# Kernel optimization log

Measured on AMD Instinct MI355X. Metric: run time of the kernel, lower is better.

## Reference

```python
import jax, jax.numpy as jnp
import numpy as np

B, S, D, H = 2, 2048, 1024, 16
HD = D // H


def setup_inputs() -> dict:
    key = jax.random.key(0)
    ks = jax.random.split(key, 9)
    x = jax.random.normal(ks[0], (B, S, D), dtype=jnp.float32)
    scale = 1.0 / np.sqrt(D)
    Wq = jax.random.normal(ks[1], (D, D), dtype=jnp.float32) * scale
    bq = jnp.zeros((D,), dtype=jnp.float32)
    Wk = jax.random.normal(ks[2], (D, D), dtype=jnp.float32) * scale
    bk = jnp.zeros((D,), dtype=jnp.float32)
    Wv = jax.random.normal(ks[3], (D, D), dtype=jnp.float32) * scale
    bv = jnp.zeros((D,), dtype=jnp.float32)
    Wo = jax.random.normal(ks[4], (D, D), dtype=jnp.float32) * scale
    bo = jnp.zeros((D,), dtype=jnp.float32)
    return {"x": x, "Wq": Wq, "bq": bq, "Wk": Wk, "bk": bk,
            "Wv": Wv, "bv": bv, "Wo": Wo, "bo": bo}


def reference(x, Wq, bq, Wk, bk, Wv, bv, Wo, bo):
    b, s, d = x.shape
    h, hd = H, HD
    # torch Linear: y = x @ W.T + b
    q = (x @ Wq.T + bq).reshape(b, s, h, hd).transpose(0, 2, 1, 3)  # (b,h,s,hd)
    k = (x @ Wk.T + bk).reshape(b, s, h, hd).transpose(0, 2, 1, 3)
    v = (x @ Wv.T + bv).reshape(b, s, h, hd).transpose(0, 2, 1, 3)
    scores = jnp.einsum('bhqd,bhkd->bhqk', q, k) / np.sqrt(hd)  # (b,h,s,s)
    # FAITHFUL to source: softmax over dim=1 (head axis), not the key axis.
    attn = jax.nn.softmax(scores, axis=1)
    # dropout is identity at inference
    out = jnp.einsum('bhqk,bhkd->bhqd', attn, v)  # (b,h,s,hd)
    out = out.transpose(0, 2, 1, 3).reshape(b, s, d)
    return out @ Wo.T + bo
```

## Files before the change

kernel.cpp:

```cpp
#include <hip/hip_runtime.h>
#include <hip/hip_bf16.h>
#include <cstdint>
#include <cstddef>


typedef __bf16 bf16x8 __attribute__((ext_vector_type(8)));
typedef __bf16 bf16x4 __attribute__((ext_vector_type(4)));
typedef _Float16 f16x4 __attribute__((ext_vector_type(4)));
typedef _Float16 f16x8 __attribute__((ext_vector_type(8)));
typedef float floatx4 __attribute__((ext_vector_type(4)));

#define S_LEN 2048
#define DIM 1024
#define NH 16
#define HD 64
#define MTOT 4096

__device__ __forceinline__ void g2l16(const void* g, void* l) {
    __builtin_amdgcn_global_load_lds(
        (const __attribute__((address_space(1))) void*)g,
        (__attribute__((address_space(3))) void*)l, 16, 0, 0);
}

__global__ void cast_f32_bf16(const float* __restrict__ s, __bf16* __restrict__ d, int n) {
    int i = (blockIdx.x * blockDim.x + threadIdx.x) * 4;
    if (i < n) {
        float4 v = *(const float4*)&s[i];
        bf16x4 o;
        o.x = (__bf16)v.x; o.y = (__bf16)v.y; o.z = (__bf16)v.z; o.w = (__bf16)v.w;
        *(bf16x4*)&d[i] = o;
    }
}

__global__ void cast_w4(const float* __restrict__ w0, const float* __restrict__ w1,
                        const float* __restrict__ w2, const float* __restrict__ w3,
                        __bf16* __restrict__ o0, __bf16* __restrict__ o1,
                        __bf16* __restrict__ o2, __bf16* __restrict__ o3, int n) {
    const float* s; __bf16* d;
    switch (blockIdx.y) {
        case 0: s = w0; d = o0; break;
        case 1: s = w1; d = o1; break;
        case 2: s = w2; d = o2; break;
        default: s = w3; d = o3; break;
    }
    int i = (blockIdx.x * blockDim.x + threadIdx.x) * 4;
    if (i < n) {
        float4 v = *(const float4*)&s[i];
        bf16x4 o;
        o.x = (__bf16)v.x; o.y = (__bf16)v.y; o.z = (__bf16)v.z; o.w = (__bf16)v.w;
        *(bf16x4*)&d[i] = o;
    }
}

__global__ __launch_bounds__(256, 4) void qkv_gemm(const __bf16* __restrict__ A,
                                                   const __bf16* __restrict__ Wq,
                                                   const __bf16* __restrict__ Wk,
                                                   const __bf16* __restrict__ Wv,
                                                   const float* __restrict__ bq,
                                                   const float* __restrict__ bk,
                                                   const float* __restrict__ bv,
                                                   __bf16* __restrict__ Qo,
                                                   __bf16* __restrict__ Ko,
                                                   _Float16* __restrict__ Vt) {
    const int tng = blockIdx.x * 64, tm = blockIdx.y * 128;
    const int wsel = tng >> 10, tn = tng & 1023;
    const __bf16* W = (wsel == 0) ? Wq : (wsel == 1) ? Wk : Wv;
    const float* bias = (wsel == 0) ? bq : (wsel == 1) ? bk : bv;
    __shared__ __bf16 As[2 * 128 * 32];
    __shared__ __bf16 Bs[2 * 64 * 32];
    const int tid = threadIdx.x, wid = tid >> 6, lane = tid & 63;
    const int l15 = lane & 15, quad = lane >> 4;
    const int wm = (wid >> 1) * 64, wn = (wid & 1) * 32;
    floatx4 acc[4][2] = {};
    for (int k0 = 0; k0 < DIM; k0 += 64) {
        __syncthreads();
#pragma unroll
        for (int i = 0; i < 4; ++i) {
            int slot = i * 256 + tid;
            int p = slot >> 9, r = (slot >> 2) & 127, c8 = (slot & 3) * 8;
            g2l16(&A[(size_t)(tm + r) * DIM + k0 + p * 32 + c8], &As[slot * 8]);
        }
#pragma unroll
        for (int i = 0; i < 2; ++i) {
            int slot = i * 256 + tid;
            int p = slot >> 8, r = (slot >> 2) & 63, c8 = (slot & 3) * 8;
            g2l16(&W[(size_t)(tn + r) * DIM + k0 + p * 32 + c8], &Bs[slot * 8]);
        }
        __syncthreads();
#pragma unroll
        for (int kc = 0; kc < 2; ++kc) {
            bf16x8 af[4], bf[2];
#pragma unroll
            for (int t = 0; t < 4; ++t)
                af[t] = *(const bf16x8*)&As[kc * 4096 + (wm + t * 16 + l15) * 32 + quad * 8];
#pragma unroll
            for (int t = 0; t < 2; ++t)
                bf[t] = *(const bf16x8*)&Bs[kc * 2048 + (wn + t * 16 + l15) * 32 + quad * 8];
#pragma unroll
            for (int im = 0; im < 4; ++im)
#pragma unroll
                for (int in = 0; in < 2; ++in)
                    acc[im][in] = __builtin_amdgcn_mfma_f32_16x16x32_bf16(af[im], bf[in], acc[im][in], 0, 0, 0);
        }
    }
    if (wsel < 2) {
        __bf16* O = wsel ? Ko : Qo;
#pragma unroll
        for (int im = 0; im < 4; ++im)
#pragma unroll
            for (int in = 0; in < 2; ++in)
#pragma unroll
                for (int r = 0; r < 4; ++r) {
                    int row = tm + wm + im * 16 + quad * 4 + r;
                    int col = tn + wn + in * 16 + l15;
                    O[(size_t)row * DIM + col] = (__bf16)(acc[im][in][r] + bias[col]);
                }
    } else {
#pragma unroll
        for (int im = 0; im < 4; ++im)
#pragma unroll
            for (int in = 0; in < 2; ++in) {
                int cv = tn + wn + in * 16 + l15;
                int row4 = tm + wm + im * 16 + quad * 4;
                float bv_ = bias[cv];
                f16x4 o;
#pragma unroll
                for (int r = 0; r < 4; ++r) o[r] = (_Float16)(acc[im][in][r] + bv_);
                *(f16x4*)&Vt[(size_t)cv * MTOT + row4] = o;
            }
    }
}

__global__ __launch_bounds__(256, 2) void gemm_out(const __bf16* __restrict__ A,
                                                   const __bf16* __restrict__ Bw,
                                                   const float* __restrict__ bias,
                                                   float* __restrict__ C) {
    const int tm = blockIdx.y * 128, tn = blockIdx.x * 64;
    __shared__ __bf16 As[2 * 128 * 32];
    __shared__ __bf16 Bs[2 * 64 * 32];
    const int tid = threadIdx.x, wid = tid >> 6, lane = tid & 63;
    const int l15 = lane & 15, quad = lane >> 4;
    const int wm = (wid >> 1) * 64, wn = (wid & 1) * 32;
    floatx4 acc[4][2] = {};
    for (int k0 = 0; k0 < DIM; k0 += 64) {
        __syncthreads();
#pragma unroll
        for (int i = 0; i < 4; ++i) {
            int slot = i * 256 + tid;
            int p = slot >> 9, r = (slot >> 2) & 127, c8 = (slot & 3) * 8;
            g2l16(&A[(size_t)(tm + r) * DIM + k0 + p * 32 + c8], &As[slot * 8]);
        }
#pragma unroll
        for (int i = 0; i < 2; ++i) {
            int slot = i * 256 + tid;
            int p = slot >> 8, r = (slot >> 2) & 63, c8 = (slot & 3) * 8;
            g2l16(&Bw[(size_t)(tn + r) * DIM + k0 + p * 32 + c8], &Bs[slot * 8]);
        }
        __syncthreads();
#pragma unroll
        for (int kc = 0; kc < 2; ++kc) {
            bf16x8 af[4], bf[2];
#pragma unroll
            for (int t = 0; t < 4; ++t)
                af[t] = *(const bf16x8*)&As[kc * 4096 + (wm + t * 16 + l15) * 32 + quad * 8];
#pragma unroll
            for (int t = 0; t < 2; ++t)
                bf[t] = *(const bf16x8*)&Bs[kc * 2048 + (wn + t * 16 + l15) * 32 + quad * 8];
#pragma unroll
            for (int im = 0; im < 4; ++im)
#pragma unroll
                for (int in = 0; in < 2; ++in)
                    acc[im][in] = __builtin_amdgcn_mfma_f32_16x16x32_bf16(af[im], bf[in], acc[im][in], 0, 0, 0);
        }
    }
#pragma unroll
    for (int im = 0; im < 4; ++im)
#pragma unroll
        for (int in = 0; in < 2; ++in)
#pragma unroll
            for (int r = 0; r < 4; ++r) {
                int row = tm + wm + im * 16 + quad * 4 + r;
                int col = tn + wn + in * 16 + l15;
                C[(size_t)row * DIM + col] = acc[im][in][r] + bias[col];
            }
}

__global__ __launch_bounds__(256, 4) void den3(const __bf16* __restrict__ Q,
                                               const __bf16* __restrict__ Km,
                                               __bf16* __restrict__ rd) {
    const int kt = blockIdx.x * 128, qt = blockIdx.y * 64, b = blockIdx.z;
    __shared__ __bf16 Ks[2 * 2 * 128 * 32];
    const int tid = threadIdx.x, wid = tid >> 6, lane = tid & 63;
    const int l15 = lane & 15, quad = lane >> 4;
    const int wq = wid * 16;
    floatx4 dsum[8] = {};
    const size_t qrow = (size_t)(b * S_LEN + qt + wq + l15) * DIM;
    for (int hh = 0; hh < 8; ++hh) {
        __syncthreads();
#pragma unroll
        for (int i = 0; i < 8; ++i) {
            int slot = i * 256 + tid;
            int hs = slot >> 10, rem = slot & 1023;
            int p = rem >> 9, r = (rem >> 2) & 127, c8 = (rem & 3) * 8;
            g2l16(&Km[(size_t)(b * S_LEN + kt + r) * DIM + (hh * 2 + hs) * HD + p * 32 + c8],
                  &Ks[slot * 8]);
        }
        __syncthreads();
#pragma unroll
        for (int hs = 0; hs < 2; ++hs) {
            int h = hh * 2 + hs;
            bf16x8 af0 = *(const bf16x8*)&Q[qrow + h * HD + quad * 8];
            bf16x8 af1 = *(const bf16x8*)&Q[qrow + h * HD + 32 + quad * 8];
#pragma unroll
            for (int n = 0; n < 8; ++n) {
                bf16x8 b0 = *(const bf16x8*)&Ks[hs * 8192 + (n * 16 + l15) * 32 + quad * 8];
                bf16x8 b1 = *(const bf16x8*)&Ks[hs * 8192 + 4096 + (n * 16 + l15) * 32 + quad * 8];
                floatx4 acc = {};
                acc = __builtin_amdgcn_mfma_f32_16x16x32_bf16(af0, b0, acc, 0, 0, 0);
                acc = __builtin_amdgcn_mfma_f32_16x16x32_bf16(af1, b1, acc, 0, 0, 0);
#pragma unroll
                for (int r = 0; r < 4; ++r) dsum[n][r] += __expf(acc[r] * 0.125f);
            }
        }
    }
#pragma unroll
    for (int n = 0; n < 8; ++n)
#pragma unroll
        for (int r = 0; r < 4; ++r) {
            int q = qt + wq + quad * 4 + r;
            int k = kt + n * 16 + l15;
            rd[(size_t)(b * S_LEN + q) * S_LEN + k] = (__bf16)(1.0f / dsum[n][r]);
        }
}

__global__ __launch_bounds__(256, 4) void attn3(const __bf16* __restrict__ Q,
                                                const __bf16* __restrict__ Km,
                                                const _Float16* __restrict__ Vt,
                                                const __bf16* __restrict__ rd,
                                                __bf16* __restrict__ AO) {
    const int qt = blockIdx.x * 64, h = blockIdx.y, b = blockIdx.z;
    __shared__ __bf16 Ks[2 * 128 * 32];
    __shared__ _Float16 Vts[64 * 136];
    const int tid = threadIdx.x, wid = tid >> 6, lane = tid & 63;
    const int l15 = lane & 15, quad = lane >> 4;
    const int wq = wid * 16;
    const size_t qrow = (size_t)(b * S_LEN + qt + wq + l15) * DIM + h * HD;
    bf16x8 qf0 = *(const bf16x8*)&Q[qrow + quad * 8];
    bf16x8 qf1 = *(const bf16x8*)&Q[qrow + 32 + quad * 8];
    const __bf16* rdrow = &rd[(size_t)(b * S_LEN + qt + wq + l15) * S_LEN];
    floatx4 oacc[4] = {};
    for (int kt = 0; kt < S_LEN; kt += 128) {
        __syncthreads();
#pragma unroll
        for (int i = 0; i < 4; ++i) {
            int slot = i * 256 + tid;
            int p = slot >> 9, r = (slot >> 2) & 127, c8 = (slot & 3) * 8;
            g2l16(&Km[(size_t)(b * S_LEN + kt + r) * DIM + h * HD + p * 32 + c8], &Ks[slot * 8]);
        }
#pragma unroll
        for (int i = 0; i < 4; ++i) {
            int slot = i * 256 + tid;
            int r = slot >> 4, c = (slot & 15) * 8;
            *(f16x8*)&Vts[r * 136 + c] =
                *(const f16x8*)&Vt[(size_t)(h * HD + r) * MTOT + b * S_LEN + kt + c];
        }
        __syncthreads();
#pragma unroll
        for (int mp = 0; mp < 8; ++mp) {
            bf16x8 kf0 = *(const bf16x8*)&Ks[(mp * 16 + l15) * 32 + quad * 8];
            bf16x8 kf1 = *(const bf16x8*)&Ks[4096 + (mp * 16 + l15) * 32 + quad * 8];
            floatx4 s = {};
            s = __builtin_amdgcn_mfma_f32_16x16x32_bf16(kf0, qf0, s, 0, 0, 0);
            s = __builtin_amdgcn_mfma_f32_16x16x32_bf16(kf1, qf1, s, 0, 0, 0);
            bf16x4 rv = *(const bf16x4*)&rdrow[kt + mp * 16 + quad * 4];
            f16x4 pa;
#pragma unroll
            for (int r = 0; r < 4; ++r)
                pa[r] = (_Float16)(__expf(s[r] * 0.125f) * (float)rv[r]);
#pragma unroll
            for (int n = 0; n < 4; ++n) {
                f16x4 vb = *(const f16x4*)&Vts[(n * 16 + l15) * 136 + mp * 16 + quad * 4];
                oacc[n] = __builtin_amdgcn_mfma_f32_16x16x16f16(pa, vb, oacc[n], 0, 0, 0);
            }
        }
    }
#pragma unroll
    for (int n = 0; n < 4; ++n)
#pragma unroll
        for (int r = 0; r < 4; ++r) {
            int row = qt + wq + quad * 4 + r;
            int col = h * HD + n * 16 + l15;
            AO[(size_t)(b * S_LEN + row) * DIM + col] = (__bf16)oacc[n][r];
        }
}

extern "C" void kernel_launch(void* const* d_in, const int* in_sizes, int n_in,
                              void* d_out, int out_size, void* d_ws, size_t ws_size,
                              hipStream_t stream) {
    const float* x  = (const float*)d_in[0];
    const float* Wq = (const float*)d_in[1];
    const float* bq = (const float*)d_in[2];
    const float* Wk = (const float*)d_in[3];
    const float* bk = (const float*)d_in[4];
    const float* Wv = (const float*)d_in[5];
    const float* bv = (const float*)d_in[6];
    const float* Wo = (const float*)d_in[7];
    const float* bo = (const float*)d_in[8];
    float* out = (float*)d_out;

    char* ws = (char*)d_ws;
    const size_t MB = 1u << 20;
    __bf16*    xb  = (__bf16*)(ws);
    __bf16*    Wqb = (__bf16*)(ws + 8 * MB);
    __bf16*    Wkb = (__bf16*)(ws + 10 * MB);
    __bf16*    Wvb = (__bf16*)(ws + 12 * MB);
    __bf16*    Wob = (__bf16*)(ws + 14 * MB);
    __bf16*    Qb  = (__bf16*)(ws + 16 * MB);
    __bf16*    Kb  = (__bf16*)(ws + 24 * MB);
    _Float16*  VtH = (_Float16*)(ws + 32 * MB);
    __bf16*    rd  = (__bf16*)(ws + 40 * MB);
    __bf16*    AOb = (__bf16*)(ws + 56 * MB);

    cast_f32_bf16<<<4096, 256, 0, stream>>>(x, xb, MTOT * DIM);
    cast_w4<<<dim3(1024, 4), 256, 0, stream>>>(Wq, Wk, Wv, Wo, Wqb, Wkb, Wvb, Wob, DIM * DIM);

    qkv_gemm<<<dim3(48, 32), 256, 0, stream>>>(xb, Wqb, Wkb, Wvb, bq, bk, bv, Qb, Kb, VtH);

    den3<<<dim3(S_LEN / 128, S_LEN / 64, 2), 256, 0, stream>>>(Qb, Kb, rd);

    attn3<<<dim3(S_LEN / 64, NH, 2), 256, 0, stream>>>(Qb, Kb, VtH, rd, AOb);

    gemm_out<<<dim3(DIM / 64, MTOT / 128), 256, 0, stream>>>(AOb, Wob, bo, out);
}
```

Baseline: 282.4 us.

## Split attention over key halves, retile GEMMs, use exp2, fp16 output projection

```diff
diff --git a/kernel.cpp b/kernel.cpp
--- a/kernel.cpp
+++ b/kernel.cpp
@@ -15,6 +15,9 @@
 #define NH 16
 #define HD 64
 #define MTOT 4096
+#define C_EXP 0.1803368801111244f
+
+__device__ __forceinline__ float fast_exp2(float x) { return __builtin_amdgcn_exp2f(x); }
 
 __device__ __forceinline__ void g2l16(const void* g, void* l) {
     __builtin_amdgcn_global_load_lds(
@@ -35,24 +38,29 @@
 __global__ void cast_w4(const float* __restrict__ w0, const float* __restrict__ w1,
                         const float* __restrict__ w2, const float* __restrict__ w3,
                         __bf16* __restrict__ o0, __bf16* __restrict__ o1,
-                        __bf16* __restrict__ o2, __bf16* __restrict__ o3, int n) {
+                        __bf16* __restrict__ o2, _Float16* __restrict__ o3, int n) {
+    int i = (blockIdx.x * blockDim.x + threadIdx.x) * 4;
+    if (i >= n) return;
+    if (blockIdx.y == 3) {
+        float4 v = *(const float4*)&w3[i];
+        f16x4 o;
+        o[0] = (_Float16)v.x; o[1] = (_Float16)v.y; o[2] = (_Float16)v.z; o[3] = (_Float16)v.w;
+        *(f16x4*)&o3[i] = o;
+        return;
+    }
     const float* s; __bf16* d;
     switch (blockIdx.y) {
         case 0: s = w0; d = o0; break;
         case 1: s = w1; d = o1; break;
-        case 2: s = w2; d = o2; break;
-        default: s = w3; d = o3; break;
-    }
-    int i = (blockIdx.x * blockDim.x + threadIdx.x) * 4;
-    if (i < n) {
-        float4 v = *(const float4*)&s[i];
-        bf16x4 o;
-        o.x = (__bf16)v.x; o.y = (__bf16)v.y; o.z = (__bf16)v.z; o.w = (__bf16)v.w;
-        *(bf16x4*)&d[i] = o;
-    }
-}
-
-__global__ __launch_bounds__(256, 4) void qkv_gemm(const __bf16* __restrict__ A,
+        default: s = w2; d = o2; break;
+    }
+    float4 v = *(const float4*)&s[i];
+    bf16x4 o;
+    o.x = (__bf16)v.x; o.y = (__bf16)v.y; o.z = (__bf16)v.z; o.w = (__bf16)v.w;
+    *(bf16x4*)&d[i] = o;
+}
+
+__global__ __launch_bounds__(256, 2) void qkv_gemm(const __bf16* __restrict__ A,
                                                    const __bf16* __restrict__ Wq,
                                                    const __bf16* __restrict__ Wk,
                                                    const __bf16* __restrict__ Wv,
@@ -62,53 +70,44 @@
                                                    __bf16* __restrict__ Qo,
                                                    __bf16* __restrict__ Ko,
                                                    _Float16* __restrict__ Vt) {
-    const int tng = blockIdx.x * 64, tm = blockIdx.y * 128;
+    const int tng = blockIdx.x * 128, tm = blockIdx.y * 128;
     const int wsel = tng >> 10, tn = tng & 1023;
     const __bf16* W = (wsel == 0) ? Wq : (wsel == 1) ? Wk : Wv;
     const float* bias = (wsel == 0) ? bq : (wsel == 1) ? bk : bv;
-    __shared__ __bf16 As[2 * 128 * 32];
-    __shared__ __bf16 Bs[2 * 64 * 32];
+    __shared__ __bf16 As[128 * 32];
+    __shared__ __bf16 Bs[128 * 32];
     const int tid = threadIdx.x, wid = tid >> 6, lane = tid & 63;
     const int l15 = lane & 15, quad = lane >> 4;
-    const int wm = (wid >> 1) * 64, wn = (wid & 1) * 32;
-    floatx4 acc[4][2] = {};
-    for (int k0 = 0; k0 < DIM; k0 += 64) {
-        __syncthreads();
-#pragma unroll
-        for (int i = 0; i < 4; ++i) {
-            int slot = i * 256 + tid;
-            int p = slot >> 9, r = (slot >> 2) & 127, c8 = (slot & 3) * 8;
-            g2l16(&A[(size_t)(tm + r) * DIM + k0 + p * 32 + c8], &As[slot * 8]);
-        }
+    const int wm = (wid >> 1) * 64, wn = (wid & 1) * 64;
+    floatx4 acc[4][4] = {};
+    for (int k0 = 0; k0 < DIM; k0 += 32) {
+        __syncthreads();
 #pragma unroll
         for (int i = 0; i < 2; ++i) {
             int slot = i * 256 + tid;
-            int p = slot >> 8, r = (slot >> 2) & 63, c8 = (slot & 3) * 8;
-            g2l16(&W[(size_t)(tn + r) * DIM + k0 + p * 32 + c8], &Bs[slot * 8]);
-        }
-        __syncthreads();
-#pragma unroll
-        for (int kc = 0; kc < 2; ++kc) {
-            bf16x8 af[4], bf[2];
-#pragma unroll
-            for (int t = 0; t < 4; ++t)
-                af[t] = *(const bf16x8*)&As[kc * 4096 + (wm + t * 16 + l15) * 32 + quad * 8];
-#pragma unroll
-            for (int t = 0; t < 2; ++t)
-                bf[t] = *(const bf16x8*)&Bs[kc * 2048 + (wn + t * 16 + l15) * 32 + quad * 8];
-#pragma unroll
-            for (int im = 0; im < 4; ++im)
-#pragma unroll
-                for (int in = 0; in < 2; ++in)
-                    acc[im][in] = __builtin_amdgcn_mfma_f32_16x16x32_bf16(af[im], bf[in], acc[im][in], 0, 0, 0);
-        }
+            int r = slot >> 2, c8 = (slot & 3) * 8;
+            g2l16(&A[(size_t)(tm + r) * DIM + k0 + c8], &As[slot * 8]);
+            g2l16(&W[(size_t)(tn + r) * DIM + k0 + c8], &Bs[slot * 8]);
+        }
+        __syncthreads();
+        bf16x8 af[4], bf[4];
+#pragma unroll
+        for (int t = 0; t < 4; ++t) {
+            af[t] = *(const bf16x8*)&As[(wm + t * 16 + l15) * 32 + quad * 8];
+            bf[t] = *(const bf16x8*)&Bs[(wn + t * 16 + l15) * 32 + quad * 8];
+        }
+#pragma unroll
+        for (int im = 0; im < 4; ++im)
+#pragma unroll
+            for (int in = 0; in < 4; ++in)
+                acc[im][in] = __builtin_amdgcn_mfma_f32_16x16x32_bf16(af[im], bf[in], acc[im][in], 0, 0, 0);
     }
     if (wsel < 2) {
         __bf16* O = wsel ? Ko : Qo;
 #pragma unroll
         for (int im = 0; im < 4; ++im)
 #pragma unroll
-            for (int in = 0; in < 2; ++in)
+            for (int in = 0; in < 4; ++in)
 #pragma unroll
                 for (int r = 0; r < 4; ++r) {
                     int row = tm + wm + im * 16 + quad * 4 + r;
@@ -119,7 +118,7 @@
 #pragma unroll
         for (int im = 0; im < 4; ++im)
 #pragma unroll
-            for (int in = 0; in < 2; ++in) {
+            for (int in = 0; in < 4; ++in) {
                 int cv = tn + wn + in * 16 + l15;
                 int row4 = tm + wm + im * 16 + quad * 4;
                 float bv_ = bias[cv];
@@ -131,77 +130,24 @@
     }
 }
 
-__global__ __launch_bounds__(256, 2) void gemm_out(const __bf16* __restrict__ A,
-                                                   const __bf16* __restrict__ Bw,
-                                                   const float* __restrict__ bias,
-                                                   float* __restrict__ C) {
-    const int tm = blockIdx.y * 128, tn = blockIdx.x * 64;
-    __shared__ __bf16 As[2 * 128 * 32];
-    __shared__ __bf16 Bs[2 * 64 * 32];
-    const int tid = threadIdx.x, wid = tid >> 6, lane = tid & 63;
-    const int l15 = lane & 15, quad = lane >> 4;
-    const int wm = (wid >> 1) * 64, wn = (wid & 1) * 32;
-    floatx4 acc[4][2] = {};
-    for (int k0 = 0; k0 < DIM; k0 += 64) {
-        __syncthreads();
-#pragma unroll
-        for (int i = 0; i < 4; ++i) {
-            int slot = i * 256 + tid;
-            int p = slot >> 9, r = (slot >> 2) & 127, c8 = (slot & 3) * 8;
-            g2l16(&A[(size_t)(tm + r) * DIM + k0 + p * 32 + c8], &As[slot * 8]);
-        }
-#pragma unroll
-        for (int i = 0; i < 2; ++i) {
-            int slot = i * 256 + tid;
-            int p = slot >> 8, r = (slot >> 2) & 63, c8 = (slot & 3) * 8;
-            g2l16(&Bw[(size_t)(tn + r) * DIM + k0 + p * 32 + c8], &Bs[slot * 8]);
-        }
-        __syncthreads();
-#pragma unroll
-        for (int kc = 0; kc < 2; ++kc) {
-            bf16x8 af[4], bf[2];
-#pragma unroll
-            for (int t = 0; t < 4; ++t)
-                af[t] = *(const bf16x8*)&As[kc * 4096 + (wm + t * 16 + l15) * 32 + quad * 8];
-#pragma unroll
-            for (int t = 0; t < 2; ++t)
-                bf[t] = *(const bf16x8*)&Bs[kc * 2048 + (wn + t * 16 + l15) * 32 + quad * 8];
-#pragma unroll
-            for (int im = 0; im < 4; ++im)
-#pragma unroll
-                for (int in = 0; in < 2; ++in)
-                    acc[im][in] = __builtin_amdgcn_mfma_f32_16x16x32_bf16(af[im], bf[in], acc[im][in], 0, 0, 0);
-        }
-    }
-#pragma unroll
-    for (int im = 0; im < 4; ++im)
-#pragma unroll
-        for (int in = 0; in < 2; ++in)
-#pragma unroll
-            for (int r = 0; r < 4; ++r) {
-                int row = tm + wm + im * 16 + quad * 4 + r;
-                int col = tn + wn + in * 16 + l15;
-                C[(size_t)row * DIM + col] = acc[im][in][r] + bias[col];
-            }
-}
-
-__global__ __launch_bounds__(256, 4) void den3(const __bf16* __restrict__ Q,
+__global__ __launch_bounds__(256, 8) void den4(const __bf16* __restrict__ Q,
                                                const __bf16* __restrict__ Km,
                                                __bf16* __restrict__ rd) {
-    const int kt = blockIdx.x * 128, qt = blockIdx.y * 64, b = blockIdx.z;
-    __shared__ __bf16 Ks[2 * 2 * 128 * 32];
+    const int kt = blockIdx.x * 64, qt = blockIdx.y * 64, b = blockIdx.z;
+    __shared__ __bf16 Ks[2 * 2 * 64 * 32];
     const int tid = threadIdx.x, wid = tid >> 6, lane = tid & 63;
     const int l15 = lane & 15, quad = lane >> 4;
     const int wq = wid * 16;
-    floatx4 dsum[8] = {};
+    floatx4 dsum[4] = {};
     const size_t qrow = (size_t)(b * S_LEN + qt + wq + l15) * DIM;
     for (int hh = 0; hh < 8; ++hh) {
         __syncthreads();
 #pragma unroll
-        for (int i = 0; i < 8; ++i) {
-            int slot = i * 256 + tid;
-            int hs = slot >> 10, rem = slot & 1023;
-            int p = rem >> 9, r = (rem >> 2) & 127, c8 = (rem & 3) * 8;
+        for (int i = 0; i < 4; ++i) {
+            int slot = i * 256 + tid;
+            int hs = slot >> 9, rem = slot & 511;
+            int p = rem >> 8, rem2 = rem & 255;
+            int r = rem2 >> 2, c8 = (rem2 & 3) * 8;
             g2l16(&Km[(size_t)(b * S_LEN + kt + r) * DIM + (hh * 2 + hs) * HD + p * 32 + c8],
                   &Ks[slot * 8]);
         }
@@ -212,19 +158,19 @@
             bf16x8 af0 = *(const bf16x8*)&Q[qrow + h * HD + quad * 8];
             bf16x8 af1 = *(const bf16x8*)&Q[qrow + h * HD + 32 + quad * 8];
 #pragma unroll
-            for (int n = 0; n < 8; ++n) {
-                bf16x8 b0 = *(const bf16x8*)&Ks[hs * 8192 + (n * 16 + l15) * 32 + quad * 8];
-                bf16x8 b1 = *(const bf16x8*)&Ks[hs * 8192 + 4096 + (n * 16 + l15) * 32 + quad * 8];
+            for (int n = 0; n < 4; ++n) {
+                bf16x8 b0 = *(const bf16x8*)&Ks[hs * 4096 + (n * 16 + l15) * 32 + quad * 8];
+                bf16x8 b1 = *(const bf16x8*)&Ks[hs * 4096 + 2048 + (n * 16 + l15) * 32 + quad * 8];
                 floatx4 acc = {};
                 acc = __builtin_amdgcn_mfma_f32_16x16x32_bf16(af0, b0, acc, 0, 0, 0);
                 acc = __builtin_amdgcn_mfma_f32_16x16x32_bf16(af1, b1, acc, 0, 0, 0);
 #pragma unroll
-                for (int r = 0; r < 4; ++r) dsum[n][r] += __expf(acc[r] * 0.125f);
-            }
-        }
-    }
-#pragma unroll
-    for (int n = 0; n < 8; ++n)
+                for (int r = 0; r < 4; ++r) dsum[n][r] += fast_exp2(acc[r] * C_EXP);
+            }
+        }
+    }
+#pragma unroll
+    for (int n = 0; n < 4; ++n)
 #pragma unroll
         for (int r = 0; r < 4; ++r) {
             int q = qt + wq + quad * 4 + r;
@@ -233,14 +179,16 @@
         }
 }
 
-__global__ __launch_bounds__(256, 4) void attn3(const __bf16* __restrict__ Q,
+__global__ __launch_bounds__(256, 8) void attn4(const __bf16* __restrict__ Q,
                                                 const __bf16* __restrict__ Km,
                                                 const _Float16* __restrict__ Vt,
                                                 const __bf16* __restrict__ rd,
-                                                __bf16* __restrict__ AO) {
-    const int qt = blockIdx.x * 64, h = blockIdx.y, b = blockIdx.z;
-    __shared__ __bf16 Ks[2 * 128 * 32];
-    __shared__ _Float16 Vts[64 * 136];
+                                                _Float16* __restrict__ AO1,
+                                                _Float16* __restrict__ AO2) {
+    const int qt = (blockIdx.x >> 1) * 64, ks = blockIdx.x & 1;
+    const int h = blockIdx.y, b = blockIdx.z;
+    __shared__ __bf16 Ks[2 * 64 * 32];
+    __shared__ _Float16 Vts[64 * 72];
     const int tid = threadIdx.x, wid = tid >> 6, lane = tid & 63;
     const int l15 = lane & 15, quad = lane >> 4;
     const int wq = wid * 16;
@@ -249,26 +197,28 @@
     bf16x8 qf1 = *(const bf16x8*)&Q[qrow + 32 + quad * 8];
     const __bf16* rdrow = &rd[(size_t)(b * S_LEN + qt + wq + l15) * S_LEN];
     floatx4 oacc[4] = {};
-    for (int kt = 0; kt < S_LEN; kt += 128) {
-        __syncthreads();
-#pragma unroll
-        for (int i = 0; i < 4; ++i) {
-            int slot = i * 256 + tid;
-            int p = slot >> 9, r = (slot >> 2) & 127, c8 = (slot & 3) * 8;
+    const int kt0 = ks * (S_LEN / 2), kt1 = kt0 + S_LEN / 2;
+    for (int kt = kt0; kt < kt1; kt += 64) {
+        __syncthreads();
+#pragma unroll
+        for (int i = 0; i < 2; ++i) {
+            int slot = i * 256 + tid;
+            int p = slot >> 8, rem = slot & 255;
+            int r = rem >> 2, c8 = (rem & 3) * 8;
             g2l16(&Km[(size_t)(b * S_LEN + kt + r) * DIM + h * HD + p * 32 + c8], &Ks[slot * 8]);
         }
 #pragma unroll
-        for (int i = 0; i < 4; ++i) {
-            int slot = i * 256 + tid;
-            int r = slot >> 4, c = (slot & 15) * 8;
-            *(f16x8*)&Vts[r * 136 + c] =
+        for (int i = 0; i < 2; ++i) {
+            int slot = i * 256 + tid;
+            int r = slot >> 3, c = (slot & 7) * 8;
+            *(f16x8*)&Vts[r * 72 + c] =
                 *(const f16x8*)&Vt[(size_t)(h * HD + r) * MTOT + b * S_LEN + kt + c];
         }
         __syncthreads();
 #pragma unroll
-        for (int mp = 0; mp < 8; ++mp) {
+        for (int mp = 0; mp < 4; ++mp) {
             bf16x8 kf0 = *(const bf16x8*)&Ks[(mp * 16 + l15) * 32 + quad * 8];
-            bf16x8 kf1 = *(const bf16x8*)&Ks[4096 + (mp * 16 + l15) * 32 + quad * 8];
+            bf16x8 kf1 = *(const bf16x8*)&Ks[2048 + (mp * 16 + l15) * 32 + quad * 8];
             floatx4 s = {};
             s = __builtin_amdgcn_mfma_f32_16x16x32_bf16(kf0, qf0, s, 0, 0, 0);
             s = __builtin_amdgcn_mfma_f32_16x16x32_bf16(kf1, qf1, s, 0, 0, 0);
@@ -276,22 +226,87 @@
             f16x4 pa;
 #pragma unroll
             for (int r = 0; r < 4; ++r)
-                pa[r] = (_Float16)(__expf(s[r] * 0.125f) * (float)rv[r]);
+                pa[r] = (_Float16)(fast_exp2(s[r] * C_EXP) * (float)rv[r]);
 #pragma unroll
             for (int n = 0; n < 4; ++n) {
-                f16x4 vb = *(const f16x4*)&Vts[(n * 16 + l15) * 136 + mp * 16 + quad * 4];
+                f16x4 vb = *(const f16x4*)&Vts[(n * 16 + l15) * 72 + mp * 16 + quad * 4];
                 oacc[n] = __builtin_amdgcn_mfma_f32_16x16x16f16(pa, vb, oacc[n], 0, 0, 0);
             }
         }
     }
+    _Float16* AO = ks ? AO2 : AO1;
 #pragma unroll
     for (int n = 0; n < 4; ++n)
 #pragma unroll
         for (int r = 0; r < 4; ++r) {
             int row = qt + wq + quad * 4 + r;
             int col = h * HD + n * 16 + l15;
-            AO[(size_t)(b * S_LEN + row) * DIM + col] = (__bf16)oacc[n][r];
-        }
+            AO[(size_t)(b * S_LEN + row) * DIM + col] = (_Float16)oacc[n][r];
+        }
+}
+
+__global__ __launch_bounds__(256, 2) void gemm_out2(const _Float16* __restrict__ A1,
+                                                    const _Float16* __restrict__ A2,
+                                                    const _Float16* __restrict__ Bw,
+                                                    const float* __restrict__ bias,
+                                                    float* __restrict__ C) {
+    const int tm = blockIdx.y * 128, tn = blockIdx.x * 64;
+    __shared__ _Float16 As1[2 * 128 * 32];
+    __shared__ _Float16 As2[2 * 128 * 32];
+    __shared__ _Float16 Bs[2 * 64 * 32];
+    const int tid = threadIdx.x, wid = tid >> 6, lane = tid & 63;
+    const int l15 = lane & 15, quad = lane >> 4;
+    const int wm = (wid >> 1) * 64, wn = (wid & 1) * 32;
+    floatx4 acc[4][2] = {};
+    for (int k0 = 0; k0 < DIM; k0 += 64) {
+        __syncthreads();
+#pragma unroll
+        for (int i = 0; i < 4; ++i) {
+            int slot = i * 256 + tid;
+            int p = slot >> 9, rem = slot & 511;
+            int r = rem >> 2, c8 = (rem & 3) * 8;
+            size_t ga = (size_t)(tm + r) * DIM + k0 + p * 32 + c8;
+            g2l16(&A1[ga], &As1[slot * 8]);
+            g2l16(&A2[ga], &As2[slot * 8]);
+        }
+#pragma unroll
+        for (int i = 0; i < 2; ++i) {
+            int slot = i * 256 + tid;
+            int p = slot >> 8, rem = slot & 255;
+            int r = rem >> 2, c8 = (rem & 3) * 8;
+            g2l16(&Bw[(size_t)(tn + r) * DIM + k0 + p * 32 + c8], &Bs[slot * 8]);
+        }
+        __syncthreads();
+#pragma unroll
+        for (int kc = 0; kc < 2; ++kc) {
+            f16x8 af[4], bf[2];
+#pragma unroll
+            for (int t = 0; t < 4; ++t) {
+                int off = kc * 4096 + (wm + t * 16 + l15) * 32 + quad * 8;
+                f16x8 a1 = *(const f16x8*)&As1[off];
+                f16x8 a2 = *(const f16x8*)&As2[off];
+                af[t] = a1 + a2;
+            }
+#pragma unroll
+            for (int t = 0; t < 2; ++t)
+                bf[t] = *(const f16x8*)&Bs[kc * 2048 + (wn + t * 16 + l15) * 32 + quad * 8];
+#pragma unroll
+            for (int im = 0; im < 4; ++im)
+#pragma unroll
+                for (int in = 0; in < 2; ++in)
+                    acc[im][in] = __builtin_amdgcn_mfma_f32_16x16x32_f16(af[im], bf[in], acc[im][in], 0, 0, 0);
+        }
+    }
+#pragma unroll
+    for (int im = 0; im < 4; ++im)
+#pragma unroll
+        for (int in = 0; in < 2; ++in)
+#pragma unroll
+            for (int r = 0; r < 4; ++r) {
+                int row = tm + wm + im * 16 + quad * 4 + r;
+                int col = tn + wn + in * 16 + l15;
+                C[(size_t)row * DIM + col] = acc[im][in][r] + bias[col];
+            }
 }
 
 extern "C" void kernel_launch(void* const* d_in, const int* in_sizes, int n_in,
@@ -314,21 +329,22 @@
     __bf16*    Wqb = (__bf16*)(ws + 8 * MB);
     __bf16*    Wkb = (__bf16*)(ws + 10 * MB);
     __bf16*    Wvb = (__bf16*)(ws + 12 * MB);
-    __bf16*    Wob = (__bf16*)(ws + 14 * MB);
+    _Float16*  Wof = (_Float16*)(ws + 14 * MB);
     __bf16*    Qb  = (__bf16*)(ws + 16 * MB);
     __bf16*    Kb  = (__bf16*)(ws + 24 * MB);
     _Float16*  VtH = (_Float16*)(ws + 32 * MB);
     __bf16*    rd  = (__bf16*)(ws + 40 * MB);
-    __bf16*    AOb = (__bf16*)(ws + 56 * MB);
+    _Float16*  AO1 = (_Float16*)(ws + 56 * MB);
+    _Float16*  AO2 = (_Float16*)(ws + 64 * MB);
 
     cast_f32_bf16<<<4096, 256, 0, stream>>>(x, xb, MTOT * DIM);
-    cast_w4<<<dim3(1024, 4), 256, 0, stream>>>(Wq, Wk, Wv, Wo, Wqb, Wkb, Wvb, Wob, DIM * DIM);
-
-    qkv_gemm<<<dim3(48, 32), 256, 0, stream>>>(xb, Wqb, Wkb, Wvb, bq, bk, bv, Qb, Kb, VtH);
-
-    den3<<<dim3(S_LEN / 128, S_LEN / 64, 2), 256, 0, stream>>>(Qb, Kb, rd);
-
-    attn3<<<dim3(S_LEN / 64, NH, 2), 256, 0, stream>>>(Qb, Kb, VtH, rd, AOb);
-
-    gemm_out<<<dim3(DIM / 64, MTOT / 128), 256, 0, stream>>>(AOb, Wob, bo, out);
-}
+    cast_w4<<<dim3(1024, 4), 256, 0, stream>>>(Wq, Wk, Wv, Wo, Wqb, Wkb, Wvb, Wof, DIM * DIM);
+
+    qkv_gemm<<<dim3(24, 32), 256, 0, stream>>>(xb, Wqb, Wkb, Wvb, bq, bk, bv, Qb, Kb, VtH);
+
+    den4<<<dim3(S_LEN / 64, S_LEN / 64, 2), 256, 0, stream>>>(Qb, Kb, rd);
+
+    attn4<<<dim3((S_LEN / 64) * 2, NH, 2), 256, 0, stream>>>(Qb, Kb, VtH, rd, AO1, AO2);
+
+    gemm_out2<<<dim3(DIM / 64, MTOT / 128), 256, 0, stream>>>(AO1, AO2, Wof, bo, out);
+}
```

After: 289.3 us. 2.5% more time.
